# Kernel tuning notes

Hardware: AMD Instinct MI355X
Metric: run time of the kernel (lower is better)

## Reference

```python
import jax, jax.numpy as jnp
import numpy as np

EPS_BN = 1e-5  # torch BatchNorm1d default eps
EPS_W = 1e-8   # dist reciprocal eps from source


def _bn_relu(x, gamma, beta):
    # x: [B, C, N]; training-mode batchnorm (biased var over B and N per channel)
    mean = jnp.mean(x, axis=(0, 2), keepdims=True)
    var = jnp.mean((x - mean) ** 2, axis=(0, 2), keepdims=True)
    xn = (x - mean) * jax.lax.rsqrt(var + EPS_BN)
    return jax.nn.relu(xn * gamma[None, :, None] + beta[None, :, None])


def setup_inputs() -> dict:
    key = jax.random.key(0)
    ks = jax.random.split(key, 12)
    B, N, S, D = 2, 16384, 4096, 256
    mlp = [256, 256]
    in_ch = 2 * D
    inp = {
        'xyz1': jax.random.normal(ks[0], (B, 3, N), jnp.float32),
        'xyz2': jax.random.normal(ks[1], (B, 3, S), jnp.float32),
        'points1': jax.random.normal(ks[2], (B, D, N), jnp.float32),
        'points2': jax.random.normal(ks[3], (B, D, S), jnp.float32),
    }
    last = in_ch
    for i, out in enumerate(mlp):
        inp[f'W{i}'] = jax.random.normal(ks[4 + 2 * i], (out, last), jnp.float32) * (1.0 / np.sqrt(last))
        inp[f'b{i}'] = jnp.zeros((out,), jnp.float32)
        inp[f'g{i}'] = jnp.ones((out,), jnp.float32)
        inp[f'be{i}'] = jnp.zeros((out,), jnp.float32)
        last = out
    return inp


def reference(xyz1, xyz2, points1, points2, W0, b0, g0, be0, W1, b1, g1, be1):
    B = xyz1.shape[0]
    p1 = jnp.swapaxes(xyz1, 1, 2)      # [B, N, 3]
    p2 = jnp.swapaxes(xyz2, 1, 2)      # [B, S, 3]
    f2 = jnp.swapaxes(points2, 1, 2)   # [B, S, D]

    # square_distance: ||a||^2 + ||b||^2 - 2 a.b  -> [B, N, S]
    d = (jnp.sum(p1 * p1, -1)[:, :, None]
         + jnp.sum(p2 * p2, -1)[:, None, :]
         - 2.0 * jnp.einsum('bnc,bsc->bns', p1, p2))

    # 3 nearest neighbors (same math as full sort + [:, :, :3])
    neg_top, idx = jax.lax.top_k(-d, 3)       # [B, N, 3]
    dists = -neg_top
    w = 1.0 / (dists + EPS_W)
    w = w / jnp.sum(w, axis=2, keepdims=True)  # [B, N, 3]

    # gather neighbor features: [B, N, 3, D]
    gathered = f2[jnp.arange(B)[:, None, None], idx]
    interp = jnp.sum(gathered * w[..., None], axis=2)   # [B, N, D]

    # concat skip features along channels -> [B, D1+D2, N]
    new_points = jnp.concatenate([points1, jnp.swapaxes(interp, 1, 2)], axis=1)

    # 1x1 conv + BN(train) + ReLU stack
    for W, b, g, be in ((W0, b0, g0, be0), (W1, b1, g1, be1)):
        new_points = _bn_relu(jnp.einsum('oc,bcn->bon', W, new_points) + b[None, :, None], g, be)
    return new_points
```

## Files before the change

### kernel.cpp

```cpp
#include <hip/hip_runtime.h>

#define NCHUNK 16

typedef __attribute__((ext_vector_type(8))) short bf16x8;
typedef __attribute__((ext_vector_type(4))) float f32x4;

__device__ __forceinline__ unsigned short f2bf(float f){
  union { float f; unsigned u; } v; v.f = f;
  unsigned u = v.u;
  u += 0x7FFFu + ((u >> 16) & 1u);
  return (unsigned short)(u >> 16);
}

__device__ __forceinline__ float bf2f(unsigned short h){
  union { unsigned u; float f; } v; v.u = ((unsigned)h) << 16;
  return v.f;
}

__device__ __forceinline__ void gl_lds16(const void* g, void* l){
  __builtin_amdgcn_global_load_lds((const __attribute__((address_space(1))) unsigned*)g,
                                   (__attribute__((address_space(3))) unsigned*)l, 16, 0, 0);
}

__device__ __forceinline__ void ins3(float d, int s,
    float& m0, float& m1, float& m2, int& i0, int& i1, int& i2){
  bool c0 = d < m0, c1 = d < m1, c2 = d < m2;
  float om0 = m0, om1 = m1;
  m0 = fminf(om0, d);
  m1 = __builtin_amdgcn_fmed3f(om0, om1, d);
  m2 = __builtin_amdgcn_fmed3f(om1, m2, d);
  int j1 = c0 ? i0 : s;
  int j2 = c1 ? i1 : s;
  i0 = c0 ? s  : i0;
  i1 = c1 ? j1 : i1;
  i2 = c2 ? j2 : i2;
}

__global__ __launch_bounds__(256) void k_convert_w(const float* __restrict__ W0, const float* __restrict__ W1,
                            unsigned short* __restrict__ W0b, unsigned short* __restrict__ W1b,
                            const float* __restrict__ xyz2, float* __restrict__ p2p){
  int i = blockIdx.x*256 + threadIdx.x;
  if (i < 256*512) W0b[i] = f2bf(W0[i]);
  if (i < 256*256) W1b[i] = f2bf(W1[i]);
  if (i < 8192){
    int b = i >> 12, s = i & 4095;
    const float* px = xyz2 + (size_t)b*3*4096;
    float x = px[s], y = px[4096+s], z = px[8192+s];
    float4 o; o.x = x; o.y = y; o.z = z; o.w = x*x + y*y + z*z;
    *(float4*)(p2p + (size_t)i*4) = o;
  }
}

__global__ __launch_bounds__(256) void k_tp2(const float* __restrict__ p2, float* __restrict__ f2t){
  __shared__ float tile[64][65];
  int bx = blockIdx.x;
  int by = blockIdx.y;
  int b  = blockIdx.z;
  int t = threadIdx.x; int tx = t & 63; int ty = t >> 6;
  const float* src = p2 + ((size_t)b*256 + by*64)*4096 + bx*64;
  #pragma unroll
  for (int i = 0; i < 16; ++i){
    int c = ty*16 + i;
    tile[c][tx] = src[(size_t)c*4096 + tx];
  }
  __syncthreads();
  float* dst = f2t + ((size_t)b*4096 + (size_t)bx*64)*256 + by*64;
  #pragma unroll
  for (int i = 0; i < 16; ++i){
    int s = ty*16 + i;
    dst[(size_t)s*256 + tx] = tile[tx][s];
  }
}

__global__ __launch_bounds__(256) void k_tp1(const float* __restrict__ p1, unsigned short* __restrict__ Xt){
  __shared__ float tile[64][65];
  int bx = blockIdx.x;
  int by = blockIdx.y;
  int b  = blockIdx.z;
  int t = threadIdx.x; int tx = t & 63; int ty = t >> 6;
  const float* src = p1 + ((size_t)b*256 + by*64)*16384 + (size_t)bx*64;
  #pragma unroll
  for (int i = 0; i < 16; ++i){
    int c = ty*16 + i;
    tile[c][tx] = src[(size_t)c*16384 + tx];
  }
  __syncthreads();
  unsigned short* dst = Xt + ((size_t)b*16384 + (size_t)bx*64)*512 + by*64;
  #pragma unroll
  for (int i = 0; i < 16; ++i){
    int n = ty*16 + i;
    dst[(size_t)n*512 + tx] = f2bf(tile[tx][n]);
  }
}

__global__ __launch_bounds__(256) void k_knn(const float* __restrict__ xyz1, const float* __restrict__ p2p,
                      float* __restrict__ pd, int* __restrict__ pi){
  int b = blockIdx.z, cc = blockIdx.y;
  int n = blockIdx.x*256 + threadIdx.x;
  const float* q = xyz1 + (size_t)b*3*16384;
  float qx = q[n], qy = q[16384+n], qz = q[32768+n];
  float r1 = qx*qx + qy*qy + qz*qz;
  int s0 = cc*(4096/NCHUNK);
  const float4* cp = (const float4*)p2p + (size_t)b*4096 + s0;
  float m0=3.4e38f, m1=3.4e38f, m2=3.4e38f;
  int i0=0, i1=0, i2=0;
  for (int g = 0; g < (4096/NCHUNK)/8; ++g){
    float4 ca[8];
    #pragma unroll
    for (int u = 0; u < 8; ++u) ca[u] = cp[g*8 + u];
    #pragma unroll
    for (int u = 0; u < 8; ++u){
      float4 c = ca[u];
      float dot = qx*c.x + qy*c.y + qz*c.z;
      float d = (r1 + c.w) - 2.0f*dot;
      ins3(d, s0 + g*8 + u, m0, m1, m2, i0, i1, i2);
    }
  }
  size_t base = (((size_t)b*16384 + n)*NCHUNK + cc)*3;
  pd[base]=m0; pd[base+1]=m1; pd[base+2]=m2;
  pi[base]=i0; pi[base+1]=i1; pi[base+2]=i2;
}

__global__ __launch_bounds__(256) void k_knn_merge(const float* __restrict__ pd, const int* __restrict__ pi,
                            int* __restrict__ ki, float* __restrict__ kw){
  size_t qq = (size_t)blockIdx.x*256 + threadIdx.x;
  float d0=3.4e38f,d1=3.4e38f,d2=3.4e38f; int i0=0,i1=0,i2=0;
  size_t base = qq*NCHUNK*3;
  for (int c = 0; c < NCHUNK*3; ++c){
    float d = pd[base+c]; int s = pi[base+c];
    if (d < d2){
      if (d < d1){
        d2=d1; i2=i1;
        if (d < d0){ d1=d0; i1=i0; d0=d; i0=s; }
        else       { d1=d; i1=s; }
      } else { d2=d; i2=s; }
    }
  }
  float w0 = 1.0f/(d0+1e-8f), w1 = 1.0f/(d1+1e-8f), w2 = 1.0f/(d2+1e-8f);
  float inv = 1.0f/(w0+w1+w2);
  size_t kb = qq*3;
  ki[kb]=i0; ki[kb+1]=i1; ki[kb+2]=i2;
  kw[kb]=w0*inv; kw[kb+1]=w1*inv; kw[kb+2]=w2*inv;
}

__global__ __launch_bounds__(256) void k_interp(const float* __restrict__ f2t, const int* __restrict__ ki,
                         const float* __restrict__ kw, unsigned short* __restrict__ Xt){
  int t = threadIdx.x;
  int g = t >> 6; int lane = t & 63;
  size_t q = (size_t)blockIdx.x*4 + g;
  int b = (int)(q >> 14);
  const float* f2 = f2t + (size_t)b*4096*256;
  size_t kb = q*3;
  int i0 = ki[kb], i1 = ki[kb+1], i2 = ki[kb+2];
  float w0 = kw[kb], w1 = kw[kb+1], w2 = kw[kb+2];
  const float4 a = *(const float4*)(f2 + (size_t)i0*256 + lane*4);
  const float4 c = *(const float4*)(f2 + (size_t)i1*256 + lane*4);
  const float4 e = *(const float4*)(f2 + (size_t)i2*256 + lane*4);
  ushort4 o;
  o.x = f2bf(w0*a.x + w1*c.x + w2*e.x);
  o.y = f2bf(w0*a.y + w1*c.y + w2*e.y);
  o.z = f2bf(w0*a.z + w1*c.z + w2*e.z);
  o.w = f2bf(w0*a.w + w1*c.w + w2*e.w);
  *(ushort4*)(Xt + q*512 + 256 + lane*4) = o;
}

template<int K>
__global__ __launch_bounds__(256) void k_gemm(const unsigned short* __restrict__ A,
                       const unsigned short* __restrict__ Bm,
                       unsigned short* __restrict__ Cb,
                       float* __restrict__ psum, float* __restrict__ psq){
  __shared__ unsigned short As[128*32];
  __shared__ unsigned short Bs[128*32];
  __shared__ float redS[2][128];
  __shared__ float redQ[2][128];
  int t = threadIdx.x;
  int bo = blockIdx.x * 128;
  size_t bn = (size_t)blockIdx.y * 128;
  int w = t >> 6, l = t & 63;
  int wr = w >> 1, wc = w & 1;
  f32x4 acc[4][4] = {};

  const char* Ap = (const char*)A;
  const char* Bp = (const char*)Bm;
  int r0 = t >> 2;
  int cb = (t & 3) * 16;
  for (int k0 = 0; k0 < K; k0 += 32){
    __syncthreads();
    #pragma unroll
    for (int p = 0; p < 2; ++p){
      int off = (t + p*256)*16;
      int r = r0 + p*64;
      gl_lds16(Ap + (size_t)(bo + r)*(K*2) + (size_t)k0*2 + cb, (char*)As + off);
      gl_lds16(Bp + (bn + r)*(K*2) + (size_t)k0*2 + cb, (char*)Bs + off);
    }
    __syncthreads();
    bf16x8 af[4], bfr[4];
    int lr = l & 15, lk = (l >> 4) * 8;
    #pragma unroll
    for (int mt = 0; mt < 4; ++mt)
      af[mt] = *(const bf16x8*)(As + (wr*64 + mt*16 + lr)*32 + lk);
    #pragma unroll
    for (int nt = 0; nt < 4; ++nt)
      bfr[nt] = *(const bf16x8*)(Bs + (wc*64 + nt*16 + lr)*32 + lk);
    #pragma unroll
    for (int mt = 0; mt < 4; ++mt)
      #pragma unroll
      for (int nt = 0; nt < 4; ++nt)
        acc[mt][nt] = __builtin_amdgcn_mfma_f32_16x16x32_bf16(af[mt], bfr[nt], acc[mt][nt], 0, 0, 0);
  }
  int lo = (l >> 4) * 4, ln = l & 15;
  #pragma unroll
  for (int mt = 0; mt < 4; ++mt){
    #pragma unroll
    for (int nt = 0; nt < 4; ++nt){
      size_t n = bn + wc*64 + nt*16 + ln;
      int o = bo + wr*64 + mt*16 + lo;
      ushort4 ov;
      ov.x = f2bf(acc[mt][nt][0]); ov.y = f2bf(acc[mt][nt][1]);
      ov.z = f2bf(acc[mt][nt][2]); ov.w = f2bf(acc[mt][nt][3]);
      *(ushort4*)(Cb + n*256 + o) = ov;
    }
  }
  float ps[16], pq[16];
  #pragma unroll
  for (int mt = 0; mt < 4; ++mt){
    #pragma unroll
    for (int j = 0; j < 4; ++j){
      float s = 0.f, qv = 0.f;
      #pragma unroll
      for (int nt = 0; nt < 4; ++nt){
        float v = acc[mt][nt][j];
        s += v; qv += v*v;
      }
      ps[mt*4+j] = s; pq[mt*4+j] = qv;
    }
  }
  #pragma unroll
  for (int dlt = 1; dlt < 16; dlt <<= 1){
    #pragma unroll
    for (int i = 0; i < 16; ++i){
      ps[i] += __shfl_xor(ps[i], dlt);
      pq[i] += __shfl_xor(pq[i], dlt);
    }
  }
  if ((l & 15) == 0){
    #pragma unroll
    for (int mt = 0; mt < 4; ++mt){
      #pragma unroll
      for (int j = 0; j < 4; ++j){
        int ol = wr*64 + mt*16 + (l>>4)*4 + j;
        redS[wc][ol] = ps[mt*4+j];
        redQ[wc][ol] = pq[mt*4+j];
      }
    }
  }
  __syncthreads();
  if (t < 128){
    psum[(size_t)(bo + t)*256 + blockIdx.y] = redS[0][t] + redS[1][t];
    psq [(size_t)(bo + t)*256 + blockIdx.y] = redQ[0][t] + redQ[1][t];
  }
}

__global__ __launch_bounds__(256) void k_stats_f(const float* __restrict__ psum, const float* __restrict__ psq,
                          const float* __restrict__ gamma, const float* __restrict__ beta,
                          float* __restrict__ scale, float* __restrict__ shift){
  int o = blockIdx.x; int t = threadIdx.x;
  float s = psum[(size_t)o*256 + t];
  float q = psq [(size_t)o*256 + t];
  #pragma unroll
  for (int d = 1; d < 64; d <<= 1){
    s += __shfl_xor(s, d);
    q += __shfl_xor(q, d);
  }
  __shared__ float ls[4], lq[4];
  if ((t & 63) == 0){ ls[t>>6] = s; lq[t>>6] = q; }
  __syncthreads();
  if (t == 0){
    float S = ls[0]+ls[1]+ls[2]+ls[3];
    float Q = lq[0]+lq[1]+lq[2]+lq[3];
    const float invc = 1.0f/32768.0f;
    float mean = S*invc;
    float var = Q*invc - mean*mean;
    float sc = gamma[o]*rsqrtf(var + 1e-5f);
    scale[o] = sc;
    shift[o] = beta[o] - mean*sc;
  }
}

__global__ __launch_bounds__(256) void k_apply_y(const unsigned short* __restrict__ Cb, const float* __restrict__ scale,
                          const float* __restrict__ shift, unsigned short* __restrict__ Y){
  size_t i = (size_t)blockIdx.x*256 + threadIdx.x;
  ushort4 v = *(const ushort4*)(Cb + i*4);
  int c = (int)((i*4) & 255);
  ushort4 o;
  o.x = f2bf(fmaxf(0.f, bf2f(v.x)*scale[c]   + shift[c]));
  o.y = f2bf(fmaxf(0.f, bf2f(v.y)*scale[c+1] + shift[c+1]));
  o.z = f2bf(fmaxf(0.f, bf2f(v.z)*scale[c+2] + shift[c+2]));
  o.w = f2bf(fmaxf(0.f, bf2f(v.w)*scale[c+3] + shift[c+3]));
  *(ushort4*)(Y + i*4) = o;
}

__global__ __launch_bounds__(256) void k_bn_out(const unsigned short* __restrict__ Cb, const float* __restrict__ scale,
                         const float* __restrict__ shift, float* __restrict__ out){
  __shared__ float tile[64][65];
  int bx = blockIdx.x;
  int by = blockIdx.y;
  int b  = blockIdx.z;
  int t = threadIdx.x; int tx = t & 63; int ty = t >> 6;
  const unsigned short* src = Cb + ((size_t)b*16384 + (size_t)bx*64)*256 + by*64;
  int o = by*64 + tx;
  float sc = scale[o], sh = shift[o];
  #pragma unroll
  for (int i = 0; i < 16; ++i){
    int n = ty*16 + i;
    float v = bf2f(src[(size_t)n*256 + tx]);
    tile[n][tx] = fmaxf(0.f, v*sc + sh);
  }
  __syncthreads();
  float* dst = out + ((size_t)b*256 + by*64)*16384 + (size_t)bx*64;
  #pragma unroll
  for (int i = 0; i < 16; ++i){
    int oo = ty*16 + i;
    dst[(size_t)oo*16384 + tx] = tile[tx][oo];
  }
}

extern "C" void kernel_launch(void* const* d_in, const int* in_sizes, int n_in,
                              void* d_out, int out_size, void* d_ws, size_t ws_size,
                              hipStream_t stream){
  const float* xyz1    = (const float*)d_in[0];
  const float* xyz2    = (const float*)d_in[1];
  const float* points1 = (const float*)d_in[2];
  const float* points2 = (const float*)d_in[3];
  const float* W0  = (const float*)d_in[4];
  const float* g0  = (const float*)d_in[6];
  const float* be0 = (const float*)d_in[7];
  const float* W1  = (const float*)d_in[8];
  const float* g1  = (const float*)d_in[10];
  const float* be1 = (const float*)d_in[11];

  char* w = (char*)d_ws;
  size_t o = 0;
  float* f2t = (float*)(w + o); o += 8388608;
  float* p2p = (float*)(w + o); o += 131072;
  int*   kidx= (int*)(w + o);   o += 393216;
  float* kww = (float*)(w + o); o += 393216;
  unsigned short* W0b = (unsigned short*)(w + o); o += 262144;
  unsigned short* W1b = (unsigned short*)(w + o); o += 131072;
  float* psum = (float*)(w + o); o += 262144;
  float* psq  = (float*)(w + o); o += 262144;
  float* scale1 = (float*)(w + o); o += 1024;
  float* shift1 = (float*)(w + o); o += 1024;
  float* scale2 = (float*)(w + o); o += 1024;
  float* shift2 = (float*)(w + o); o += 1024;
  float* kpd = (float*)(w + o); o += 6291456;
  int*   kpi = (int*)(w + o);   o += 6291456;
  unsigned short* Xt = (unsigned short*)(w + o); size_t xto = o; o += 33554432;
  unsigned short* C1b = (unsigned short*)(w + o); o += 16777216;
  unsigned short* Yt  = (unsigned short*)(w + o); o += 16777216;
  unsigned short* C2b = (unsigned short*)(w + xto);

  k_convert_w<<<512, 256, 0, stream>>>(W0, W1, W0b, W1b, xyz2, p2p);
  k_tp2<<<dim3(64,4,2), 256, 0, stream>>>(points2, f2t);
  k_knn<<<dim3(64,NCHUNK,2), 256, 0, stream>>>(xyz1, p2p, kpd, kpi);
  k_knn_merge<<<128, 256, 0, stream>>>(kpd, kpi, kidx, kww);
  k_tp1<<<dim3(256,4,2), 256, 0, stream>>>(points1, Xt);
  k_interp<<<8192, 256, 0, stream>>>(f2t, kidx, kww, Xt);
  k_gemm<512><<<dim3(2,256), 256, 0, stream>>>(W0b, Xt, C1b, psum, psq);
  k_stats_f<<<256, 256, 0, stream>>>(psum, psq, g0, be0, scale1, shift1);
  k_apply_y<<<8192, 256, 0, stream>>>(C1b, scale1, shift1, Yt);
  k_gemm<256><<<dim3(2,256), 256, 0, stream>>>(W1b, Yt, C2b, psum, psq);
  k_stats_f<<<256, 256, 0, stream>>>(psum, psq, g1, be1, scale2, shift2);
  k_bn_out<<<dim3(256,4,2), 256, 0, stream>>>(C2b, scale2, shift2, (float*)d_out);
}
```

Baseline: 171.7 us.

## Split KNN into distance-only pass and threshold-pruned index pass

The KNN stage becomes two passes. The first computes only the three smallest distances per query with cheap fmed3 updates and no index tracking, then a merge derives the interpolation weights and the third-smallest distance as a threshold. A second pass recomputes distances and runs the index-tracking insert only when some lane in the wave has a distance at or below that threshold, so the expensive selects are mostly skipped. The cost is two full sweeps over candidates plus extra launches and traffic, and index selection may differ from the weights if distances tie.

```diff
diff --git a/kernel.cpp b/kernel.cpp
--- a/kernel.cpp
+++ b/kernel.cpp
@@ -20,6 +20,11 @@
 __device__ __forceinline__ void gl_lds16(const void* g, void* l){
   __builtin_amdgcn_global_load_lds((const __attribute__((address_space(1))) unsigned*)g,
                                    (__attribute__((address_space(3))) unsigned*)l, 16, 0, 0);
+}
+
+__device__ __forceinline__ float distf(float qx, float qy, float qz, float r1, float4 c){
+  float dot = qx*c.x + qy*c.y + qz*c.z;
+  return (r1 + c.w) - 2.0f*dot;
 }
 
 __device__ __forceinline__ void ins3(float d, int s,
@@ -93,8 +98,8 @@
   }
 }
 
-__global__ __launch_bounds__(256) void k_knn(const float* __restrict__ xyz1, const float* __restrict__ p2p,
-                      float* __restrict__ pd, int* __restrict__ pi){
+__global__ __launch_bounds__(256) void k_knn_d(const float* __restrict__ xyz1, const float* __restrict__ p2p,
+                        float* __restrict__ pd){
   int b = blockIdx.z, cc = blockIdx.y;
   int n = blockIdx.x*256 + threadIdx.x;
   const float* q = xyz1 + (size_t)b*3*16384;
@@ -103,6 +108,52 @@
   int s0 = cc*(4096/NCHUNK);
   const float4* cp = (const float4*)p2p + (size_t)b*4096 + s0;
   float m0=3.4e38f, m1=3.4e38f, m2=3.4e38f;
+  for (int g = 0; g < (4096/NCHUNK)/8; ++g){
+    float4 ca[8];
+    #pragma unroll
+    for (int u = 0; u < 8; ++u) ca[u] = cp[g*8 + u];
+    #pragma unroll
+    for (int u = 0; u < 8; ++u){
+      float d = distf(qx, qy, qz, r1, ca[u]);
+      m2 = __builtin_amdgcn_fmed3f(m1, m2, d);
+      m1 = __builtin_amdgcn_fmed3f(m0, m1, d);
+      m0 = fminf(m0, d);
+    }
+  }
+  size_t base = (((size_t)b*16384 + n)*NCHUNK + cc)*3;
+  pd[base]=m0; pd[base+1]=m1; pd[base+2]=m2;
+}
+
+__global__ __launch_bounds__(256) void k_merge_d(const float* __restrict__ pd,
+                          float* __restrict__ kw, float* __restrict__ d2g){
+  size_t qq = (size_t)blockIdx.x*256 + threadIdx.x;
+  float m0=3.4e38f, m1=3.4e38f, m2=3.4e38f;
+  size_t base = qq*NCHUNK*3;
+  for (int c = 0; c < NCHUNK*3; ++c){
+    float d = pd[base+c];
+    m2 = __builtin_amdgcn_fmed3f(m1, m2, d);
+    m1 = __builtin_amdgcn_fmed3f(m0, m1, d);
+    m0 = fminf(m0, d);
+  }
+  float w0 = 1.0f/(m0+1e-8f), w1 = 1.0f/(m1+1e-8f), w2 = 1.0f/(m2+1e-8f);
+  float inv = 1.0f/(w0+w1+w2);
+  size_t kb = qq*3;
+  kw[kb]=w0*inv; kw[kb+1]=w1*inv; kw[kb+2]=w2*inv;
+  d2g[qq] = m2;
+}
+
+__global__ __launch_bounds__(256) void k_knn_i(const float* __restrict__ xyz1, const float* __restrict__ p2p,
+                        const float* __restrict__ d2g,
+                        float* __restrict__ pd, int* __restrict__ pi){
+  int b = blockIdx.z, cc = blockIdx.y;
+  int n = blockIdx.x*256 + threadIdx.x;
+  const float* q = xyz1 + (size_t)b*3*16384;
+  float qx = q[n], qy = q[16384+n], qz = q[32768+n];
+  float r1 = qx*qx + qy*qy + qz*qz;
+  float thr = d2g[(size_t)b*16384 + n];
+  int s0 = cc*(4096/NCHUNK);
+  const float4* cp = (const float4*)p2p + (size_t)b*4096 + s0;
+  float m0=3.4e38f, m1=3.4e38f, m2=3.4e38f;
   int i0=0, i1=0, i2=0;
   for (int g = 0; g < (4096/NCHUNK)/8; ++g){
     float4 ca[8];
@@ -110,10 +161,10 @@
     for (int u = 0; u < 8; ++u) ca[u] = cp[g*8 + u];
     #pragma unroll
     for (int u = 0; u < 8; ++u){
-      float4 c = ca[u];
-      float dot = qx*c.x + qy*c.y + qz*c.z;
-      float d = (r1 + c.w) - 2.0f*dot;
-      ins3(d, s0 + g*8 + u, m0, m1, m2, i0, i1, i2);
+      float d = distf(qx, qy, qz, r1, ca[u]);
+      if (__builtin_expect((bool)__ballot(d <= thr), 0)){
+        ins3(d, s0 + g*8 + u, m0, m1, m2, i0, i1, i2);
+      }
     }
   }
   size_t base = (((size_t)b*16384 + n)*NCHUNK + cc)*3;
@@ -121,8 +172,8 @@
   pi[base]=i0; pi[base+1]=i1; pi[base+2]=i2;
 }
 
-__global__ __launch_bounds__(256) void k_knn_merge(const float* __restrict__ pd, const int* __restrict__ pi,
-                            int* __restrict__ ki, float* __restrict__ kw){
+__global__ __launch_bounds__(256) void k_merge_i(const float* __restrict__ pd, const int* __restrict__ pi,
+                          int* __restrict__ ki){
   size_t qq = (size_t)blockIdx.x*256 + threadIdx.x;
   float d0=3.4e38f,d1=3.4e38f,d2=3.4e38f; int i0=0,i1=0,i2=0;
   size_t base = qq*NCHUNK*3;
@@ -136,11 +187,8 @@
       } else { d2=d; i2=s; }
     }
   }
-  float w0 = 1.0f/(d0+1e-8f), w1 = 1.0f/(d1+1e-8f), w2 = 1.0f/(d2+1e-8f);
-  float inv = 1.0f/(w0+w1+w2);
   size_t kb = qq*3;
   ki[kb]=i0; ki[kb+1]=i1; ki[kb+2]=i2;
-  kw[kb]=w0*inv; kw[kb+1]=w1*inv; kw[kb+2]=w2*inv;
 }
 
 __global__ __launch_bounds__(256) void k_interp(const float* __restrict__ f2t, const int* __restrict__ ki,
@@ -345,6 +393,7 @@
   float* p2p = (float*)(w + o); o += 131072;
   int*   kidx= (int*)(w + o);   o += 393216;
   float* kww = (float*)(w + o); o += 393216;
+  float* d2g = (float*)(w + o); o += 131072;
   unsigned short* W0b = (unsigned short*)(w + o); o += 262144;
   unsigned short* W1b = (unsigned short*)(w + o); o += 131072;
   float* psum = (float*)(w + o); o += 262144;
@@ -362,8 +411,10 @@
 
   k_convert_w<<<512, 256, 0, stream>>>(W0, W1, W0b, W1b, xyz2, p2p);
   k_tp2<<<dim3(64,4,2), 256, 0, stream>>>(points2, f2t);
-  k_knn<<<dim3(64,NCHUNK,2), 256, 0, stream>>>(xyz1, p2p, kpd, kpi);
-  k_knn_merge<<<128, 256, 0, stream>>>(kpd, kpi, kidx, kww);
+  k_knn_d<<<dim3(64,NCHUNK,2), 256, 0, stream>>>(xyz1, p2p, kpd);
+  k_merge_d<<<128, 256, 0, stream>>>(kpd, kww, d2g);
+  k_knn_i<<<dim3(64,NCHUNK,2), 256, 0, stream>>>(xyz1, p2p, d2g, kpd, kpi);
+  k_merge_i<<<128, 256, 0, stream>>>(kpd, kpi, kidx);
   k_tp1<<<dim3(256,4,2), 256, 0, stream>>>(points1, Xt);
   k_interp<<<8192, 256, 0, stream>>>(f2t, kidx, kww, Xt);
   k_gemm<512><<<dim3(2,256), 256, 0, stream>>>(W0b, Xt, C1b, psum, psq);
```

Measured after the change: 179.3 us. 4.4% more time.

## Fuse BN1+ReLU into second GEMM B-load and pack KNN distance math

Applied to the files above, without the earlier changes.

Removes the separate apply kernel and the Yt intermediate buffer by applying scale/shift/ReLU to C1 while staging the B tile in the second GEMM. It also reorganizes candidate points into paired SoA records so the KNN kernel can compute two distances at once with packed float2 FMAs. This is meant to save a full bf16 read-and-write pass over the activations and to cut VALU work in KNN. In exchange, the B operand now goes through register loads rather than direct global-to-LDS loads, and the activation is recomputed per output-row block (twice).

```diff
diff --git a/kernel.cpp b/kernel.cpp
--- a/kernel.cpp
+++ b/kernel.cpp
@@ -4,6 +4,10 @@
 
 typedef __attribute__((ext_vector_type(8))) short bf16x8;
 typedef __attribute__((ext_vector_type(4))) float f32x4;
+typedef __attribute__((ext_vector_type(2))) float f32x2;
+typedef __attribute__((ext_vector_type(8))) short short8v;
+
+struct PairRec { f32x2 x, y, z, w; };
 
 __device__ __forceinline__ unsigned short f2bf(float f){
   union { float f; unsigned u; } v; v.f = f;
@@ -20,6 +24,15 @@
 __device__ __forceinline__ void gl_lds16(const void* g, void* l){
   __builtin_amdgcn_global_load_lds((const __attribute__((address_space(1))) unsigned*)g,
                                    (__attribute__((address_space(3))) unsigned*)l, 16, 0, 0);
+}
+
+__device__ __forceinline__ f32x2 pkdist(PairRec p, f32x2 qx2, f32x2 qy2, f32x2 qz2, f32x2 r12){
+  f32x2 dot = p.x * qx2;
+  dot = __builtin_elementwise_fma(p.y, qy2, dot);
+  dot = __builtin_elementwise_fma(p.z, qz2, dot);
+  f32x2 t = r12 + p.w;
+  f32x2 n2 = {-2.0f, -2.0f};
+  return __builtin_elementwise_fma(dot, n2, t);
 }
 
 __device__ __forceinline__ void ins3(float d, int s,
@@ -38,7 +51,7 @@
 
 __global__ __launch_bounds__(256) void k_convert_w(const float* __restrict__ W0, const float* __restrict__ W1,
                             unsigned short* __restrict__ W0b, unsigned short* __restrict__ W1b,
-                            const float* __restrict__ xyz2, float* __restrict__ p2p){
+                            const float* __restrict__ xyz2, float* __restrict__ p2pp){
   int i = blockIdx.x*256 + threadIdx.x;
   if (i < 256*512) W0b[i] = f2bf(W0[i]);
   if (i < 256*256) W1b[i] = f2bf(W1[i]);
@@ -46,8 +59,9 @@
     int b = i >> 12, s = i & 4095;
     const float* px = xyz2 + (size_t)b*3*4096;
     float x = px[s], y = px[4096+s], z = px[8192+s];
-    float4 o; o.x = x; o.y = y; o.z = z; o.w = x*x + y*y + z*z;
-    *(float4*)(p2p + (size_t)i*4) = o;
+    float r2 = x*x + y*y + z*z;
+    size_t base = (size_t)b*16384 + (size_t)(s >> 1)*8 + (s & 1);
+    p2pp[base+0] = x; p2pp[base+2] = y; p2pp[base+4] = z; p2pp[base+6] = r2;
   }
 }
 
@@ -93,28 +107,34 @@
   }
 }
 
-__global__ __launch_bounds__(256) void k_knn(const float* __restrict__ xyz1, const float* __restrict__ p2p,
+__global__ __launch_bounds__(256) void k_knn(const float* __restrict__ xyz1, const float* __restrict__ p2pp,
                       float* __restrict__ pd, int* __restrict__ pi){
   int b = blockIdx.z, cc = blockIdx.y;
   int n = blockIdx.x*256 + threadIdx.x;
   const float* q = xyz1 + (size_t)b*3*16384;
   float qx = q[n], qy = q[16384+n], qz = q[32768+n];
   float r1 = qx*qx + qy*qy + qz*qz;
+  f32x2 qx2 = {qx,qx}, qy2 = {qy,qy}, qz2 = {qz,qz}, r12 = {r1,r1};
+  const int NP = (4096/NCHUNK)/2;
   int s0 = cc*(4096/NCHUNK);
-  const float4* cp = (const float4*)p2p + (size_t)b*4096 + s0;
+  const PairRec* pp = (const PairRec*)p2pp + (size_t)b*2048 + cc*NP;
   float m0=3.4e38f, m1=3.4e38f, m2=3.4e38f;
   int i0=0, i1=0, i2=0;
-  for (int g = 0; g < (4096/NCHUNK)/8; ++g){
-    float4 ca[8];
-    #pragma unroll
-    for (int u = 0; u < 8; ++u) ca[u] = cp[g*8 + u];
-    #pragma unroll
-    for (int u = 0; u < 8; ++u){
-      float4 c = ca[u];
-      float dot = qx*c.x + qy*c.y + qz*c.z;
-      float d = (r1 + c.w) - 2.0f*dot;
-      ins3(d, s0 + g*8 + u, m0, m1, m2, i0, i1, i2);
-    }
+  for (int g = 0; g < NP/4; ++g){
+    PairRec pA = pp[g*4+0], pB = pp[g*4+1], pC = pp[g*4+2], pD = pp[g*4+3];
+    int sb = s0 + g*8;
+    f32x2 dA = pkdist(pA, qx2, qy2, qz2, r12);
+    ins3(dA.x, sb+0, m0,m1,m2, i0,i1,i2);
+    ins3(dA.y, sb+1, m0,m1,m2, i0,i1,i2);
+    f32x2 dB = pkdist(pB, qx2, qy2, qz2, r12);
+    ins3(dB.x, sb+2, m0,m1,m2, i0,i1,i2);
+    ins3(dB.y, sb+3, m0,m1,m2, i0,i1,i2);
+    f32x2 dC = pkdist(pC, qx2, qy2, qz2, r12);
+    ins3(dC.x, sb+4, m0,m1,m2, i0,i1,i2);
+    ins3(dC.y, sb+5, m0,m1,m2, i0,i1,i2);
+    f32x2 dD = pkdist(pD, qx2, qy2, qz2, r12);
+    ins3(dD.x, sb+6, m0,m1,m2, i0,i1,i2);
+    ins3(dD.y, sb+7, m0,m1,m2, i0,i1,i2);
   }
   size_t base = (((size_t)b*16384 + n)*NCHUNK + cc)*3;
   pd[base]=m0; pd[base+1]=m1; pd[base+2]=m2;
@@ -261,6 +281,123 @@
   }
 }
 
+__global__ __launch_bounds__(256) void k_gemm2(const unsigned short* __restrict__ A,
+                       const unsigned short* __restrict__ C1,
+                       const float* __restrict__ scale, const float* __restrict__ shift,
+                       unsigned short* __restrict__ Cb,
+                       float* __restrict__ psum, float* __restrict__ psq){
+  const int K = 256;
+  __shared__ unsigned short As[128*32];
+  __shared__ unsigned short Bs[128*32];
+  __shared__ float redS[2][128];
+  __shared__ float redQ[2][128];
+  int t = threadIdx.x;
+  int bo = blockIdx.x * 128;
+  size_t bn = (size_t)blockIdx.y * 128;
+  int w = t >> 6, l = t & 63;
+  int wr = w >> 1, wc = w & 1;
+  f32x4 acc[4][4] = {};
+
+  const char* Ap = (const char*)A;
+  int r0 = t >> 2;
+  int cb = (t & 3) * 16;
+  int ce0 = (t & 3) * 8;
+  for (int k0 = 0; k0 < K; k0 += 32){
+    int ce = k0 + ce0;
+    float4 a0 = *(const float4*)(scale+ce); float4 a1 = *(const float4*)(scale+ce+4);
+    float4 b0 = *(const float4*)(shift+ce); float4 b1 = *(const float4*)(shift+ce+4);
+    float sc[8] = {a0.x,a0.y,a0.z,a0.w,a1.x,a1.y,a1.z,a1.w};
+    float sh[8] = {b0.x,b0.y,b0.z,b0.w,b1.x,b1.y,b1.z,b1.w};
+    short8v vin[2];
+    #pragma unroll
+    for (int p = 0; p < 2; ++p){
+      int r = r0 + p*64;
+      vin[p] = *(const short8v*)(C1 + (bn + r)*256 + ce);
+    }
+    __syncthreads();
+    #pragma unroll
+    for (int p = 0; p < 2; ++p){
+      int r = r0 + p*64;
+      gl_lds16(Ap + (size_t)(bo + r)*(K*2) + (size_t)k0*2 + cb, (char*)As + (t + p*256)*16);
+    }
+    #pragma unroll
+    for (int p = 0; p < 2; ++p){
+      short8v pv;
+      #pragma unroll
+      for (int j = 0; j < 8; ++j){
+        float y = fmaxf(0.f, bf2f((unsigned short)vin[p][j])*sc[j] + sh[j]);
+        pv[j] = (short)f2bf(y);
+      }
+      *(short8v*)((char*)Bs + (t + p*256)*16) = pv;
+    }
+    __syncthreads();
+    bf16x8 af[4], bfr[4];
+    int lr = l & 15, lk = (l >> 4) * 8;
+    #pragma unroll
+    for (int mt = 0; mt < 4; ++mt)
+      af[mt] = *(const bf16x8*)(As + (wr*64 + mt*16 + lr)*32 + lk);
+    #pragma unroll
+    for (int nt = 0; nt < 4; ++nt)
+      bfr[nt] = *(const bf16x8*)(Bs + (wc*64 + nt*16 + lr)*32 + lk);
+    #pragma unroll
+    for (int mt = 0; mt < 4; ++mt)
+      #pragma unroll
+      for (int nt = 0; nt < 4; ++nt)
+        acc[mt][nt] = __builtin_amdgcn_mfma_f32_16x16x32_bf16(af[mt], bfr[nt], acc[mt][nt], 0, 0, 0);
+  }
+  int lo = (l >> 4) * 4, ln = l & 15;
+  #pragma unroll
+  for (int mt = 0; mt < 4; ++mt){
+    #pragma unroll
+    for (int nt = 0; nt < 4; ++nt){
+      size_t n = bn + wc*64 + nt*16 + ln;
+      int o = bo + wr*64 + mt*16 + lo;
+      ushort4 ov;
+      ov.x = f2bf(acc[mt][nt][0]); ov.y = f2bf(acc[mt][nt][1]);
+      ov.z = f2bf(acc[mt][nt][2]); ov.w = f2bf(acc[mt][nt][3]);
+      *(ushort4*)(Cb + n*256 + o) = ov;
+    }
+  }
+  float ps[16], pq[16];
+  #pragma unroll
+  for (int mt = 0; mt < 4; ++mt){
+    #pragma unroll
+    for (int j = 0; j < 4; ++j){
+      float s = 0.f, qv = 0.f;
+      #pragma unroll
+      for (int nt = 0; nt < 4; ++nt){
+        float v = acc[mt][nt][j];
+        s += v; qv += v*v;
+      }
+      ps[mt*4+j] = s; pq[mt*4+j] = qv;
+    }
+  }
+  #pragma unroll
+  for (int dlt = 1; dlt < 16; dlt <<= 1){
+    #pragma unroll
+    for (int i = 0; i < 16; ++i){
+      ps[i] += __shfl_xor(ps[i], dlt);
+      pq[i] += __shfl_xor(pq[i], dlt);
+    }
+  }
+  if ((l & 15) == 0){
+    #pragma unroll
+    for (int mt = 0; mt < 4; ++mt){
+      #pragma unroll
+      for (int j = 0; j < 4; ++j){
+        int ol = wr*64 + mt*16 + (l>>4)*4 + j;
+        redS[wc][ol] = ps[mt*4+j];
+        redQ[wc][ol] = pq[mt*4+j];
+      }
+    }
+  }
+  __syncthreads();
+  if (t < 128){
+    psum[(size_t)(bo + t)*256 + blockIdx.y] = redS[0][t] + redS[1][t];
+    psq [(size_t)(bo + t)*256 + blockIdx.y] = redQ[0][t] + redQ[1][t];
+  }
+}
+
 __global__ __launch_bounds__(256) void k_stats_f(const float* __restrict__ psum, const float* __restrict__ psq,
                           const float* __restrict__ gamma, const float* __restrict__ beta,
                           float* __restrict__ scale, float* __restrict__ shift){
@@ -285,19 +422,6 @@
     scale[o] = sc;
     shift[o] = beta[o] - mean*sc;
   }
-}
-
-__global__ __launch_bounds__(256) void k_apply_y(const unsigned short* __restrict__ Cb, const float* __restrict__ scale,
-                          const float* __restrict__ shift, unsigned short* __restrict__ Y){
-  size_t i = (size_t)blockIdx.x*256 + threadIdx.x;
-  ushort4 v = *(const ushort4*)(Cb + i*4);
-  int c = (int)((i*4) & 255);
-  ushort4 o;
-  o.x = f2bf(fmaxf(0.f, bf2f(v.x)*scale[c]   + shift[c]));
-  o.y = f2bf(fmaxf(0.f, bf2f(v.y)*scale[c+1] + shift[c+1]));
-  o.z = f2bf(fmaxf(0.f, bf2f(v.z)*scale[c+2] + shift[c+2]));
-  o.w = f2bf(fmaxf(0.f, bf2f(v.w)*scale[c+3] + shift[c+3]));
-  *(ushort4*)(Y + i*4) = o;
 }
 
 __global__ __launch_bounds__(256) void k_bn_out(const unsigned short* __restrict__ Cb, const float* __restrict__ scale,
@@ -342,7 +466,7 @@
   char* w = (char*)d_ws;
   size_t o = 0;
   float* f2t = (float*)(w + o); o += 8388608;
-  float* p2p = (float*)(w + o); o += 131072;
+  float* p2pp= (float*)(w + o); o += 131072;
   int*   kidx= (int*)(w + o);   o += 393216;
   float* kww = (float*)(w + o); o += 393216;
   unsigned short* W0b = (unsigned short*)(w + o); o += 262144;
@@ -357,19 +481,17 @@
   int*   kpi = (int*)(w + o);   o += 6291456;
   unsigned short* Xt = (unsigned short*)(w + o); size_t xto = o; o += 33554432;
   unsigned short* C1b = (unsigned short*)(w + o); o += 16777216;
-  unsigned short* Yt  = (unsigned short*)(w + o); o += 16777216;
   unsigned short* C2b = (unsigned short*)(w + xto);
 
-  k_convert_w<<<512, 256, 0, stream>>>(W0, W1, W0b, W1b, xyz2, p2p);
+  k_convert_w<<<512, 256, 0, stream>>>(W0, W1, W0b, W1b, xyz2, p2pp);
   k_tp2<<<dim3(64,4,2), 256, 0, stream>>>(points2, f2t);
-  k_knn<<<dim3(64,NCHUNK,2), 256, 0, stream>>>(xyz1, p2p, kpd, kpi);
+  k_knn<<<dim3(64,NCHUNK,2), 256, 0, stream>>>(xyz1, p2pp, kpd, kpi);
   k_knn_merge<<<128, 256, 0, stream>>>(kpd, kpi, kidx, kww);
   k_tp1<<<dim3(256,4,2), 256, 0, stream>>>(points1, Xt);
   k_interp<<<8192, 256, 0, stream>>>(f2t, kidx, kww, Xt);
   k_gemm<512><<<dim3(2,256), 256, 0, stream>>>(W0b, Xt, C1b, psum, psq);
   k_stats_f<<<256, 256, 0, stream>>>(psum, psq, g0, be0, scale1, shift1);
-  k_apply_y<<<8192, 256, 0, stream>>>(C1b, scale1, shift1, Yt);
-  k_gemm<256><<<dim3(2,256), 256, 0, stream>>>(W1b, Yt, C2b, psum, psq);
+  k_gemm2<<<dim3(2,256), 256, 0, stream>>>(W1b, C1b, scale1, shift1, C2b, psum, psq);
   k_stats_f<<<256, 256, 0, stream>>>(psum, psq, g1, be1, scale2, shift2);
   k_bn_out<<<dim3(256,4,2), 256, 0, stream>>>(C2b, scale2, shift2, (float*)d_out);
 }
```

Result: faster. 159.8 us (-6.9%).
